# Kernel tuning notes

Hardware: AMD Instinct MI355X
Metric: run time of the kernel (lower is better)

Reference implementation:

```python
import jax, jax.numpy as jnp
import numpy as np

# dims: batch B, seq S, model D, query heads H, kv heads KV, head_dim HD, group G
B, S, D = 2, 2048, 2048
H, KV, HD = 16, 4, 128
G = H // KV
THETA = 10000.0


def setup_inputs() -> dict:
    key = jax.random.key(0)
    ks = jax.random.split(key, 5)
    x = jax.random.normal(ks[0], (B, S, D), dtype=jnp.float32)
    # RoPE frequencies (real/imag parts of complex freqs_cis)
    inv_freq = 1.0 / (THETA ** (jnp.arange(0, HD, 2, dtype=jnp.float32) / HD))  # (HD/2,)
    t = jnp.arange(S, dtype=jnp.float32)
    freqs = jnp.outer(t, inv_freq)                      # (S, HD/2)
    freqs_cos = jnp.cos(freqs)
    freqs_sin = jnp.sin(freqs)
    # causal additive mask
    mask = jnp.where(jnp.tril(jnp.ones((S, S), dtype=bool)), 0.0, -1e9).astype(jnp.float32)
    sc = 0.02
    wq = jax.random.normal(ks[1], (D, H * HD), dtype=jnp.float32) * sc
    wk = jax.random.normal(ks[2], (D, KV * HD), dtype=jnp.float32) * sc
    wv = jax.random.normal(ks[3], (D, KV * HD), dtype=jnp.float32) * sc
    wo = jax.random.normal(ks[4], (H * HD, D), dtype=jnp.float32) * sc
    return {"x": x, "freqs_cos": freqs_cos, "freqs_sin": freqs_sin, "mask": mask,
            "wq": wq, "wk": wk, "wv": wv, "wo": wo}


def _apply_rope(x, cos, sin):
    # x: (B, S, nh, HD); cos/sin: (S, HD/2). Interleaved complex rotation.
    xr = x.reshape(*x.shape[:-1], HD // 2, 2)
    xe, xo = xr[..., 0], xr[..., 1]
    c = cos[None, :, None, :]
    s = sin[None, :, None, :]
    out_e = xe * c - xo * s
    out_o = xe * s + xo * c
    return jnp.stack([out_e, out_o], axis=-1).reshape(x.shape)


def reference(x, freqs_cos, freqs_sin, mask, wq, wk, wv, wo):
    q = (x @ wq).reshape(B, S, H, HD)
    k = (x @ wk).reshape(B, S, KV, HD)
    v = (x @ wv).reshape(B, S, KV, HD)
    q = _apply_rope(q, freqs_cos, freqs_sin)
    k = _apply_rope(k, freqs_cos, freqs_sin)
    # GQA: group query heads instead of expanding KV (same math as expand)
    qg = q.reshape(B, S, KV, G, HD)
    scale = jnp.sqrt(jnp.float32(HD))
    scores = jnp.einsum('bqkgd,bskd->bkgqs', qg, k) / scale   # (B,KV,G,S,S)
    scores = scores + mask                                     # broadcast (S,S)
    attn = jax.nn.softmax(scores, axis=-1)
    out = jnp.einsum('bkgqs,bskd->bqkgd', attn, v)             # (B,S,KV,G,HD)
    out = out.reshape(B, S, H * HD)
    return out @ wo
```

## Files before the change

kernel.cpp:

```cpp
#include <hip/hip_runtime.h>
#include <type_traits>

typedef short s8v   __attribute__((ext_vector_type(8)));
typedef float f32x4 __attribute__((ext_vector_type(4)));
typedef float f32x16 __attribute__((ext_vector_type(16)));
typedef unsigned int u32x2 __attribute__((ext_vector_type(2)));
typedef unsigned int u32x4 __attribute__((ext_vector_type(4)));

__device__ __forceinline__ unsigned short f2bf(float f) {
    unsigned int u = __builtin_bit_cast(unsigned int, f);
    u += 0x7FFF + ((u >> 16) & 1);
    return (unsigned short)(u >> 16);
}
__device__ __forceinline__ float bf2f(unsigned short b) {
    unsigned int u = ((unsigned int)b) << 16;
    return __builtin_bit_cast(float, u);
}
__device__ __forceinline__ unsigned int cvtpk(float lo, float hi) {
    unsigned int w;
    asm("v_cvt_pk_bf16_f32 %0, %1, %2" : "=v"(w) : "v"(lo), "v"(hi));
    return w;
}

__device__ __forceinline__ void gload16(const void* g, void* l) {
    __builtin_amdgcn_global_load_lds(
        (const __attribute__((address_space(1))) void*)g,
        (__attribute__((address_space(3))) void*)l, 16, 0, 0);
}

__global__ void conv_bf16(const float* __restrict__ src, unsigned short* __restrict__ dst, int n8) {
    int i = blockIdx.x * blockDim.x + threadIdx.x;
    if (i >= n8) return;
    const f32x4* s4 = (const f32x4*)src;
    f32x4 a = s4[2 * i], b = s4[2 * i + 1];
    s8v o;
    o[0] = (short)f2bf(a[0]); o[1] = (short)f2bf(a[1]);
    o[2] = (short)f2bf(a[2]); o[3] = (short)f2bf(a[3]);
    o[4] = (short)f2bf(b[0]); o[5] = (short)f2bf(b[1]);
    o[6] = (short)f2bf(b[2]); o[7] = (short)f2bf(b[3]);
    *(s8v*)(dst + (size_t)i * 8) = o;
}

__global__ void transpose_conv(const float* __restrict__ src, unsigned short* __restrict__ dst,
                               int K, int N) {
    __shared__ float tile[32][33];
    int n0 = blockIdx.x * 32, k0 = blockIdx.y * 32;
    int tx = threadIdx.x, ty = threadIdx.y;
#pragma unroll
    for (int r = 0; r < 4; ++r)
        tile[ty + r * 8][tx] = src[(size_t)(k0 + ty + r * 8) * N + n0 + tx];
    __syncthreads();
#pragma unroll
    for (int r = 0; r < 4; ++r)
        dst[(size_t)(n0 + ty + r * 8) * K + k0 + tx] = f2bf(tile[tx][ty + r * 8]);
}

__global__ void vtrans(const unsigned short* __restrict__ qkv, unsigned short* __restrict__ vt) {
    __shared__ unsigned short t[32][33];
    int s0 = blockIdx.x * 32;
    int c0 = blockIdx.y * 32;
    int tx = threadIdx.x, ty = threadIdx.y;
#pragma unroll
    for (int r = 0; r < 4; ++r)
        t[ty + r * 8][tx] = qkv[(size_t)(s0 + ty + r * 8) * 3072 + 2560 + c0 + tx];
    __syncthreads();
    int b = s0 >> 11, s = s0 & 2047;
    size_t dbase = (size_t)(b * 4 + (c0 >> 7)) * 128 + (c0 & 127);
#pragma unroll
    for (int r = 0; r < 4; ++r)
        vt[(dbase + ty + r * 8) * 2048 + s + tx] = t[tx][ty + r * 8];
}

template <typename CT>
__global__ __launch_bounds__(256)
void gemm_bt(const unsigned short* __restrict__ A, const unsigned short* __restrict__ BT,
             CT* __restrict__ C, int M, int N, int K, int ldc) {
    __shared__ unsigned short As[128 * 32];
    __shared__ unsigned short Bs[128 * 32];
    const int tid = threadIdx.x;
    const int wid = tid >> 6, lane = tid & 63;
    const int lr = lane & 15, lg = lane >> 4;
    const int brow = blockIdx.y * 128, bcol = blockIdx.x * 128;
    const int wr = wid >> 1, wc = wid & 1;
    f32x4 acc[4][4] = {};

    for (int kt = 0; kt < K; kt += 32) {
#pragma unroll
        for (int i = 0; i < 2; ++i) {
            int f = i * 256 + tid;
            int row = f >> 2;
            int col8 = (f & 3) << 3;
            gload16(A + (size_t)(brow + row) * K + kt + col8,
                    As + (size_t)(i * 256 + wid * 64) * 8);
            gload16(BT + (size_t)(bcol + row) * K + kt + col8,
                    Bs + (size_t)(i * 256 + wid * 64) * 8);
        }
        __syncthreads();
        s8v a[4], b[4];
#pragma unroll
        for (int m = 0; m < 4; ++m)
            a[m] = *(const s8v*)(As + (size_t)(wr * 64 + m * 16 + lr) * 32 + lg * 8);
#pragma unroll
        for (int n = 0; n < 4; ++n)
            b[n] = *(const s8v*)(Bs + (size_t)(wc * 64 + n * 16 + lr) * 32 + lg * 8);
#pragma unroll
        for (int m = 0; m < 4; ++m)
#pragma unroll
            for (int n = 0; n < 4; ++n)
                acc[m][n] = __builtin_amdgcn_mfma_f32_16x16x32_bf16(a[m], b[n], acc[m][n], 0, 0, 0);
        __syncthreads();
    }
#pragma unroll
    for (int m = 0; m < 4; ++m)
#pragma unroll
        for (int n = 0; n < 4; ++n)
#pragma unroll
            for (int j = 0; j < 4; ++j) {
                int r = brow + wr * 64 + m * 16 + lg * 4 + j;
                int c = bcol + wc * 64 + n * 16 + lr;
                float v = acc[m][n][j];
                if constexpr (std::is_same<CT, float>::value)
                    C[(size_t)r * ldc + c] = v;
                else
                    C[(size_t)r * ldc + c] = f2bf(v);
            }
}

__global__ void rope_kernel(unsigned short* __restrict__ qkv,
                            const float* __restrict__ fc, const float* __restrict__ fs) {
    int idx = blockIdx.x * blockDim.x + threadIdx.x;
    if (idx >= 4096 * 20 * 16) return;
    int grp = idx & 15;
    int hh = (idx >> 4) % 20;
    int row = idx / (16 * 20);
    int s = row & 2047;
    int col0 = (hh < 16 ? hh * 128 : 2048 + (hh - 16) * 128) + grp * 8;
    unsigned short* p = qkv + (size_t)row * 3072 + col0;
    s8v v = *(const s8v*)p;
    const float* cc = fc + (size_t)s * 64 + grp * 4;
    const float* ss = fs + (size_t)s * 64 + grp * 4;
#pragma unroll
    for (int j = 0; j < 4; ++j) {
        float xe = bf2f((unsigned short)v[2 * j]);
        float xo = bf2f((unsigned short)v[2 * j + 1]);
        float c = cc[j], sn = ss[j];
        v[2 * j]     = (short)f2bf(xe * c - xo * sn);
        v[2 * j + 1] = (short)f2bf(xe * sn + xo * c);
    }
    *(s8v*)p = v;
}

__global__ __launch_bounds__(256)
void attn_kernel(const unsigned short* __restrict__ qkv,
                 const unsigned short* __restrict__ vtg,
                 unsigned short* __restrict__ out) {
    constexpr int S = 2048;
    __shared__ unsigned short Ks[2][64 * 128];
    __shared__ unsigned short Vs[2][128 * 64];
    const int tid = threadIdx.x, lane = tid & 63, wid = tid >> 6;
    const int l31 = lane & 31, h2 = lane >> 5;
    const int lsw = l31 & 7;
    const int g8 = blockIdx.x & 7;
    const int b = g8 >> 2, kvh = g8 & 3;
    const int qi = 63 - (blockIdx.x >> 3);
    const int h = kvh * 4 + wid;
    const int qw = qi * 32;
    const int qq = qw + l31;
    const size_t rs = 3072;
    const float rscale = 0.08838834764831845f;

    const unsigned short* Qp = qkv + (size_t)(b * S + qw) * rs + h * 128 + h2 * 8;
    const unsigned short* Kbase = qkv + (size_t)(b * S) * rs + 2048 + kvh * 128;
    const unsigned short* Vtg = vtg + (size_t)((b * 4 + kvh) * 128) * S;

    s8v qf[8];
#pragma unroll
    for (int kk = 0; kk < 8; ++kk)
        qf[kk] = *(const s8v*)(Qp + (size_t)l31 * rs + kk * 16);

    f32x16 acc[4] = {};
    float m_run = -1e30f, l_run = 0.f;
    const int nt = (qi >> 1) + 1;

    auto stage = [&](int t, int bufi) {
        const int kb64 = t * 64;
#pragma unroll
        for (int i = 0; i < 4; ++i) {
            int c = i * 256 + tid;
            int key = c >> 4, d8 = c & 15;
            gload16(Kbase + (size_t)(kb64 + key) * rs + ((d8 ^ (key & 7)) << 3),
                    &Ks[bufi][(size_t)c * 8]);
        }
#pragma unroll
        for (int i = 0; i < 4; ++i) {
            int c = i * 256 + tid;
            int d = c >> 3, k8 = c & 7;
            gload16(Vtg + (size_t)d * S + kb64 + ((k8 ^ (d & 7)) << 3),
                    &Vs[bufi][(size_t)c * 8]);
        }
    };

    int cur = 0;
    stage(0, 0);
    __syncthreads();

    for (int t = 0; t < nt; ++t) {
        if (t + 1 < nt) stage(t + 1, cur ^ 1);
        const int kb64 = t * 64;
        const char* Kb = (const char*)&Ks[cur][0];
        const char* Vb = (const char*)&Vs[cur][0];

        s8v kf0[8], kf1[8];
#pragma unroll
        for (int kk = 0; kk < 8; ++kk)
            kf0[kk] = *(const s8v*)(Kb + l31 * 256 + (((2 * kk + h2) ^ lsw) << 4));
#pragma unroll
        for (int kk = 0; kk < 8; ++kk)
            kf1[kk] = *(const s8v*)(Kb + (32 + l31) * 256 + (((2 * kk + h2) ^ lsw) << 4));
        s8v vf[4][4];
#pragma unroll
        for (int kb = 0; kb < 4; ++kb)
#pragma unroll
            for (int dblk = 0; dblk < 4; ++dblk)
                vf[kb][dblk] = *(const s8v*)(Vb + (32 * dblk + l31) * 128 +
                                             (((2 * kb + h2) ^ lsw) << 4));

        f32x16 sacc0 = {}, sacc1 = {};
        __builtin_amdgcn_s_setprio(1);
#pragma unroll
        for (int kk = 0; kk < 8; ++kk)
            sacc0 = __builtin_amdgcn_mfma_f32_32x32x16_bf16(kf0[kk], qf[kk], sacc0, 0, 0, 0);
#pragma unroll
        for (int kk = 0; kk < 8; ++kk)
            sacc1 = __builtin_amdgcn_mfma_f32_32x32x16_bf16(kf1[kk], qf[kk], sacc1, 0, 0, 0);
        __builtin_amdgcn_s_setprio(0);

        float sv[32];
#pragma unroll
        for (int g = 0; g < 2; ++g)
#pragma unroll
            for (int r = 0; r < 16; ++r) {
                int key = kb64 + 32 * g + (r & 3) + 8 * (r >> 2) + 4 * h2;
                float s = (g ? sacc1[r] : sacc0[r]) * rscale;
                sv[g * 16 + r] = (key <= qq) ? s : -1e30f;
            }

        float mx = sv[0];
#pragma unroll
        for (int i = 1; i < 32; ++i) mx = fmaxf(mx, sv[i]);
        mx = fmaxf(mx, __shfl_xor(mx, 32));
        if (!__all(mx - m_run <= 8.f)) {
            float mn = fmaxf(m_run, mx);
            float alpha = __expf(m_run - mn);
            m_run = mn;
            l_run *= alpha;
#pragma unroll
            for (int dblk = 0; dblk < 4; ++dblk)
#pragma unroll
                for (int r = 0; r < 16; ++r) acc[dblk][r] *= alpha;
        }
        float ps = 0.f;
#pragma unroll
        for (int i = 0; i < 32; ++i) {
            float e = __expf(sv[i] - m_run);
            sv[i] = e;
            ps += e;
        }
        ps += __shfl_xor(ps, 32);
        l_run += ps;

        unsigned int pw[4][4];
#pragma unroll
        for (int g = 0; g < 2; ++g) {
            unsigned int w[8];
#pragma unroll
            for (int j = 0; j < 8; ++j)
                w[j] = cvtpk(sv[g * 16 + 2 * j], sv[g * 16 + 2 * j + 1]);
#pragma unroll
            for (int u = 0; u < 2; ++u) {
                unsigned int t0 = (unsigned)__shfl_xor((int)w[4 * u + 0], 32);
                unsigned int t1 = (unsigned)__shfl_xor((int)w[4 * u + 1], 32);
                unsigned int t2 = (unsigned)__shfl_xor((int)w[4 * u + 2], 32);
                unsigned int t3 = (unsigned)__shfl_xor((int)w[4 * u + 3], 32);
                pw[2 * g + u][0] = h2 ? t2 : w[4 * u + 0];
                pw[2 * g + u][1] = h2 ? t3 : w[4 * u + 1];
                pw[2 * g + u][2] = h2 ? w[4 * u + 2] : t0;
                pw[2 * g + u][3] = h2 ? w[4 * u + 3] : t1;
            }
        }

        __builtin_amdgcn_s_setprio(1);
#pragma unroll
        for (int kb = 0; kb < 4; ++kb) {
            u32x4 wv;
            wv[0] = pw[kb][0]; wv[1] = pw[kb][1]; wv[2] = pw[kb][2]; wv[3] = pw[kb][3];
            s8v pf = __builtin_bit_cast(s8v, wv);
#pragma unroll
            for (int dblk = 0; dblk < 4; ++dblk)
                acc[dblk] = __builtin_amdgcn_mfma_f32_32x32x16_bf16(vf[kb][dblk], pf, acc[dblk], 0, 0, 0);
        }
        __builtin_amdgcn_s_setprio(0);

        __syncthreads();
        cur ^= 1;
    }

    float inv = 1.f / l_run;
    unsigned short* Op = out + (size_t)(b * S + qq) * 2048 + h * 128 + 4 * h2;
#pragma unroll
    for (int dblk = 0; dblk < 4; ++dblk)
#pragma unroll
        for (int s = 0; s < 4; ++s) {
            u32x2 wv;
            wv[0] = cvtpk(acc[dblk][4 * s + 0] * inv, acc[dblk][4 * s + 1] * inv);
            wv[1] = cvtpk(acc[dblk][4 * s + 2] * inv, acc[dblk][4 * s + 3] * inv);
            *(u32x2*)(Op + 32 * dblk + 8 * s) = wv;
        }
}

extern "C" void kernel_launch(void* const* d_in, const int* in_sizes, int n_in,
                              void* d_out, int out_size, void* d_ws, size_t ws_size,
                              hipStream_t stream) {
    const float* x  = (const float*)d_in[0];
    const float* fc = (const float*)d_in[1];
    const float* fs = (const float*)d_in[2];
    const float* wq = (const float*)d_in[4];
    const float* wk = (const float*)d_in[5];
    const float* wv = (const float*)d_in[6];
    const float* wo = (const float*)d_in[7];
    float* out = (float*)d_out;

    char* ws = (char*)d_ws;
    unsigned short* xb    = (unsigned short*)ws;
    unsigned short* wqkvT = (unsigned short*)(ws + 16777216);
    unsigned short* woT   = (unsigned short*)(ws + 16777216 + 12582912);
    unsigned short* qkvb  = (unsigned short*)(ws + 16777216 + 12582912 + 8388608);
    unsigned short* attnb = xb;
    unsigned short* vtb   = wqkvT;

    conv_bf16<<<4096, 256, 0, stream>>>(x, xb, 1048576);
    dim3 tb(32, 8);
    transpose_conv<<<dim3(64, 64), tb, 0, stream>>>(wq, wqkvT, 2048, 2048);
    transpose_conv<<<dim3(16, 64), tb, 0, stream>>>(wk, wqkvT + (size_t)2048 * 2048, 2048, 512);
    transpose_conv<<<dim3(16, 64), tb, 0, stream>>>(wv, wqkvT + (size_t)2560 * 2048, 2048, 512);
    transpose_conv<<<dim3(64, 64), tb, 0, stream>>>(wo, woT, 2048, 2048);
    gemm_bt<unsigned short><<<dim3(24, 32), 256, 0, stream>>>(xb, wqkvT, qkvb, 4096, 3072, 2048, 3072);
    rope_kernel<<<5120, 256, 0, stream>>>(qkvb, fc, fs);
    vtrans<<<dim3(128, 16), tb, 0, stream>>>(qkvb, vtb);
    attn_kernel<<<512, 256, 0, stream>>>(qkvb, vtb, attnb);
    gemm_bt<float><<<dim3(16, 32), 256, 0, stream>>>(attnb, woT, out, 4096, 2048, 2048, 2048);
}
```

Measured before the change: 258.9 us.

## Fuse RoPE into QKV GEMM epilogue, merge QKV weight transposes, rebalance attention order

Applies the rotary embedding inside the QKV projection GEMM epilogue. The even/odd partner value comes from a lane shuffle, so the separate rope kernel's read-modify-write pass over the bf16 QKV buffer is gone. The three Q/K/V weight transpose-convert launches are merged into one kernel, and the attention block-to-query-tile mapping is changed so heavy and light causal tiles are interleaved across the grid. RoPE is now applied to fp32 accumulators before bf16 rounding, which changes rounding slightly; the epilogue also gains extra cos/sin loads and shuffles.

```diff
diff --git a/kernel.cpp b/kernel.cpp
--- a/kernel.cpp
+++ b/kernel.cpp
@@ -55,6 +55,24 @@
         dst[(size_t)(n0 + ty + r * 8) * K + k0 + tx] = f2bf(tile[tx][ty + r * 8]);
 }
 
+__global__ void transpose_conv_qkv(const float* __restrict__ wq, const float* __restrict__ wk,
+                                   const float* __restrict__ wv, unsigned short* __restrict__ dst) {
+    __shared__ float tile[32][33];
+    int n0 = blockIdx.x * 32, k0 = blockIdx.y * 32;
+    const float* src; int sc, N;
+    if (n0 < 2048)      { src = wq; sc = n0;        N = 2048; }
+    else if (n0 < 2560) { src = wk; sc = n0 - 2048; N = 512;  }
+    else                { src = wv; sc = n0 - 2560; N = 512;  }
+    int tx = threadIdx.x, ty = threadIdx.y;
+#pragma unroll
+    for (int r = 0; r < 4; ++r)
+        tile[ty + r * 8][tx] = src[(size_t)(k0 + ty + r * 8) * N + sc + tx];
+    __syncthreads();
+#pragma unroll
+    for (int r = 0; r < 4; ++r)
+        dst[(size_t)(n0 + ty + r * 8) * 2048 + k0 + tx] = f2bf(tile[tx][ty + r * 8]);
+}
+
 __global__ void vtrans(const unsigned short* __restrict__ qkv, unsigned short* __restrict__ vt) {
     __shared__ unsigned short t[32][33];
     int s0 = blockIdx.x * 32;
@@ -71,10 +89,11 @@
         vt[(dbase + ty + r * 8) * 2048 + s + tx] = t[tx][ty + r * 8];
 }
 
-template <typename CT>
+template <typename CT, bool ROPE>
 __global__ __launch_bounds__(256)
 void gemm_bt(const unsigned short* __restrict__ A, const unsigned short* __restrict__ BT,
-             CT* __restrict__ C, int M, int N, int K, int ldc) {
+             CT* __restrict__ C, const float* __restrict__ fc, const float* __restrict__ fs,
+             int M, int N, int K, int ldc) {
     __shared__ unsigned short As[128 * 32];
     __shared__ unsigned short Bs[128 * 32];
     const int tid = threadIdx.x;
@@ -119,35 +138,19 @@
                 int r = brow + wr * 64 + m * 16 + lg * 4 + j;
                 int c = bcol + wc * 64 + n * 16 + lr;
                 float v = acc[m][n][j];
+                if constexpr (ROPE) {
+                    float vp = __shfl_xor(v, 1);
+                    if (c < 2560) {
+                        int fi = ((r & 2047) << 6) + ((c & 127) >> 1);
+                        float cs = fc[fi], sn = fs[fi];
+                        v = (lr & 1) ? (vp * sn + v * cs) : (v * cs - vp * sn);
+                    }
+                }
                 if constexpr (std::is_same<CT, float>::value)
                     C[(size_t)r * ldc + c] = v;
                 else
                     C[(size_t)r * ldc + c] = f2bf(v);
             }
-}
-
-__global__ void rope_kernel(unsigned short* __restrict__ qkv,
-                            const float* __restrict__ fc, const float* __restrict__ fs) {
-    int idx = blockIdx.x * blockDim.x + threadIdx.x;
-    if (idx >= 4096 * 20 * 16) return;
-    int grp = idx & 15;
-    int hh = (idx >> 4) % 20;
-    int row = idx / (16 * 20);
-    int s = row & 2047;
-    int col0 = (hh < 16 ? hh * 128 : 2048 + (hh - 16) * 128) + grp * 8;
-    unsigned short* p = qkv + (size_t)row * 3072 + col0;
-    s8v v = *(const s8v*)p;
-    const float* cc = fc + (size_t)s * 64 + grp * 4;
-    const float* ss = fs + (size_t)s * 64 + grp * 4;
-#pragma unroll
-    for (int j = 0; j < 4; ++j) {
-        float xe = bf2f((unsigned short)v[2 * j]);
-        float xo = bf2f((unsigned short)v[2 * j + 1]);
-        float c = cc[j], sn = ss[j];
-        v[2 * j]     = (short)f2bf(xe * c - xo * sn);
-        v[2 * j + 1] = (short)f2bf(xe * sn + xo * c);
-    }
-    *(s8v*)p = v;
 }
 
 __global__ __launch_bounds__(256)
@@ -162,7 +165,8 @@
     const int lsw = l31 & 7;
     const int g8 = blockIdx.x & 7;
     const int b = g8 >> 2, kvh = g8 & 3;
-    const int qi = 63 - (blockIdx.x >> 3);
+    const int k = blockIdx.x >> 3;
+    const int qi = (k < 32) ? (63 - k) : (k - 32);
     const int h = kvh * 4 + wid;
     const int qw = qi * 32;
     const int qq = qw + l31;
@@ -340,13 +344,12 @@
 
     conv_bf16<<<4096, 256, 0, stream>>>(x, xb, 1048576);
     dim3 tb(32, 8);
-    transpose_conv<<<dim3(64, 64), tb, 0, stream>>>(wq, wqkvT, 2048, 2048);
-    transpose_conv<<<dim3(16, 64), tb, 0, stream>>>(wk, wqkvT + (size_t)2048 * 2048, 2048, 512);
-    transpose_conv<<<dim3(16, 64), tb, 0, stream>>>(wv, wqkvT + (size_t)2560 * 2048, 2048, 512);
+    transpose_conv_qkv<<<dim3(96, 64), tb, 0, stream>>>(wq, wk, wv, wqkvT);
     transpose_conv<<<dim3(64, 64), tb, 0, stream>>>(wo, woT, 2048, 2048);
-    gemm_bt<unsigned short><<<dim3(24, 32), 256, 0, stream>>>(xb, wqkvT, qkvb, 4096, 3072, 2048, 3072);
-    rope_kernel<<<5120, 256, 0, stream>>>(qkvb, fc, fs);
+    gemm_bt<unsigned short, true><<<dim3(24, 32), 256, 0, stream>>>(
+        xb, wqkvT, qkvb, fc, fs, 4096, 3072, 2048, 3072);
     vtrans<<<dim3(128, 16), tb, 0, stream>>>(qkvb, vtb);
     attn_kernel<<<512, 256, 0, stream>>>(qkvb, vtb, attnb);
-    gemm_bt<float><<<dim3(16, 32), 256, 0, stream>>>(attnb, woT, out, 4096, 2048, 2048, 2048);
-}
+    gemm_bt<float, false><<<dim3(16, 32), 256, 0, stream>>>(
+        attnb, woT, out, nullptr, nullptr, 4096, 2048, 2048, 2048);
+}
```

Measured after the change: 282.0 us. +8.9%, slower.
